# Kernel tuning notes

Measured on AMD Instinct MI355X. Metric: run time of the kernel, lower is better.

The kernel has to match this reference:

```python
import jax, jax.numpy as jnp
import numpy as np

N_HEADS = 16
N_KV_HEADS = 4
HEAD_DIM = 128
ROPE_BASE = 10000.0


def _rms_norm(x):
    eps = jnp.asarray(jnp.finfo(x.dtype).eps, x.dtype)
    return x * jax.lax.rsqrt(jnp.mean(x * x, axis=-1, keepdims=True) + eps)


def _rope_tables(T, dtype):
    d = HEAD_DIM
    inv_freq = 1.0 / (ROPE_BASE ** (jnp.arange(0, d, 2, dtype=jnp.float32) / d))
    freqs = jnp.outer(jnp.arange(T, dtype=jnp.float32), inv_freq)  # [T, d/2]
    return jnp.cos(freqs).astype(dtype), jnp.sin(freqs).astype(dtype)


def _apply_rope(x, cos, sin):
    # x: [B, H, T, D]; cos/sin: [T, D/2]
    d = x.shape[-1] // 2
    x1, x2 = x[..., :d], x[..., d:]
    return jnp.concatenate((x1 * cos + x2 * sin, -x1 * sin + x2 * cos), axis=-1)


def setup_inputs() -> dict:
    key = jax.random.key(0)
    ks = jax.random.split(key, 5)
    B, T, C = 2, 2048, 2048
    kv_dim = N_KV_HEADS * HEAD_DIM
    s = 0.02
    return {
        "x": jax.random.normal(ks[0], (B, T, C), jnp.float32),
        "Wq": jax.random.normal(ks[1], (C, C), jnp.float32) * s,
        "Wk": jax.random.normal(ks[2], (kv_dim, C), jnp.float32) * s,
        "Wv": jax.random.normal(ks[3], (kv_dim, C), jnp.float32) * s,
        "Wo": jax.random.normal(ks[4], (C, C), jnp.float32) * s,
    }


def reference(x, Wq, Wk, Wv, Wo):
    B, T, C = x.shape
    g = N_HEADS // N_KV_HEADS

    # QKV projections (torch Linear: x @ W.T), split into heads -> [B, H, T, D]
    q = (x @ Wq.T).reshape(B, T, N_HEADS, HEAD_DIM).transpose(0, 2, 1, 3)
    k = (x @ Wk.T).reshape(B, T, N_KV_HEADS, HEAD_DIM).transpose(0, 2, 1, 3)
    v = (x @ Wv.T).reshape(B, T, N_KV_HEADS, HEAD_DIM).transpose(0, 2, 1, 3)

    # QK RMSNorm (no learned weight)
    q, k = _rms_norm(q), _rms_norm(k)

    # RoPE
    cos, sin = _rope_tables(T, q.dtype)
    q, k = _apply_rope(q, cos, sin), _apply_rope(k, cos, sin)

    # GQA: expand kv heads
    k = jnp.repeat(k, g, axis=1)
    v = jnp.repeat(v, g, axis=1)

    # causal SDPA
    scale = 1.0 / jnp.sqrt(jnp.asarray(HEAD_DIM, q.dtype))
    scores = jnp.einsum("bhqd,bhkd->bhqk", q, k) * scale
    mask = jnp.tril(jnp.ones((T, T), bool))
    scores = jnp.where(mask, scores, jnp.asarray(-jnp.inf, scores.dtype))
    att = jax.nn.softmax(scores, axis=-1)
    y = jnp.einsum("bhqk,bhkd->bhqd", att, v)

    y = y.transpose(0, 2, 1, 3).reshape(B, T, C)
    return y @ Wo.T
```

## Files before the change

kernel.cpp:

```cpp
#include <hip/hip_runtime.h>
#include <hip/hip_bf16.h>
#include <cstdint>
#include <math.h>

#define DEVINL __device__ __forceinline__

typedef __attribute__((ext_vector_type(8))) __bf16 bf16x8;
typedef __attribute__((ext_vector_type(4))) float floatx4;

constexpr int TB = 2;
constexpr int TT = 2048;
constexpr int TC = 2048;
constexpr int NH = 16, NKV = 4, HD = 128;
constexpr int MR = TB * TT;
constexpr int NQ = NH * HD;
constexpr int NK = NKV * HD;
constexpr int NQKV = NQ + 2 * NK;

DEVINL unsigned bfbits(float f) {
  unsigned u = __builtin_bit_cast(unsigned, f);
  return (u + 0x7FFFu + ((u >> 16) & 1u)) >> 16;
}
DEVINL int pk2(float a, float b) {
  union { __hip_bfloat162 h; int i; } u;
  u.h = __float22bfloat162_rn(float2{a, b});
  return u.i;
}
DEVINL void gl_lds16(const __hip_bfloat16* g, __hip_bfloat16* l) {
  __builtin_amdgcn_global_load_lds(
      (const __attribute__((address_space(1))) unsigned int*)g,
      (__attribute__((address_space(3))) unsigned int*)l, 16, 0, 0);
}
DEVINL floatx4 mfma16(bf16x8 a, bf16x8 b, floatx4 c) {
  return __builtin_amdgcn_mfma_f32_16x16x32_bf16(a, b, c, 0, 0, 0);
}
DEVINL void cstore(float* p, float v) { *p = v; }
DEVINL void cstore(__hip_bfloat16* p, float v) { *(unsigned short*)p = (unsigned short)bfbits(v); }

__global__ __launch_bounds__(256) void k_cvt5(
    const float* __restrict__ s0, const float* __restrict__ s1,
    const float* __restrict__ s2, const float* __restrict__ s3,
    const float* __restrict__ s4,
    __hip_bfloat16* __restrict__ d0, __hip_bfloat16* __restrict__ d1,
    __hip_bfloat16* __restrict__ d2, __hip_bfloat16* __restrict__ d3,
    __hip_bfloat16* __restrict__ d4) {
  const float* s;
  __hip_bfloat16* d;
  int n;
  switch (blockIdx.y) {
    case 0: s = s0; d = d0; n = MR * TC; break;
    case 1: s = s1; d = d1; n = NQ * TC; break;
    case 2: s = s2; d = d2; n = NK * TC; break;
    case 3: s = s3; d = d3; n = NK * TC; break;
    default: s = s4; d = d4; n = TC * TC; break;
  }
  int i = (blockIdx.x * 256 + threadIdx.x) * 4;
  if (i >= n) return;
  float4 v = *(const float4*)(s + i);
  ushort4 o;
  o.x = (unsigned short)bfbits(v.x);
  o.y = (unsigned short)bfbits(v.y);
  o.z = (unsigned short)bfbits(v.z);
  o.w = (unsigned short)bfbits(v.w);
  *(ushort4*)(d + i) = o;
}

template <typename OUT_T>
__global__ __launch_bounds__(256, 2) void k_gemm_bt(
    const __hip_bfloat16* __restrict__ A, const __hip_bfloat16* __restrict__ B,
    OUT_T* __restrict__ C, int M, int N, int K) {
  __shared__ __align__(16) __hip_bfloat16 As[128 * 32];
  __shared__ __align__(16) __hip_bfloat16 Bs[128 * 32];
  const int tid = threadIdx.x;
  const int lane = tid & 63, w = tid >> 6;
  const int q15 = lane & 15, quad = lane >> 4;
  const int wm = w >> 1, wn = w & 1;
  const int tm = blockIdx.y, tn = blockIdx.x;

  const int r0 = tid >> 2, c0 = (tid & 3) * 8;
  const __hip_bfloat16* a0 = A + (size_t)(tm * 128 + r0) * K + c0;
  const __hip_bfloat16* a1 = A + (size_t)(tm * 128 + r0 + 64) * K + c0;
  const __hip_bfloat16* b0 = B + (size_t)(tn * 128 + r0) * K + c0;
  const __hip_bfloat16* b1 = B + (size_t)(tn * 128 + r0 + 64) * K + c0;
  __hip_bfloat16* lA0 = As + (tid & ~63) * 8;
  __hip_bfloat16* lA1 = As + 2048 + (tid & ~63) * 8;
  __hip_bfloat16* lB0 = Bs + (tid & ~63) * 8;
  __hip_bfloat16* lB1 = Bs + 2048 + (tid & ~63) * 8;

  floatx4 acc[4][4] = {};
  for (int k0 = 0; k0 < K; k0 += 32) {
    __syncthreads();
    gl_lds16(a0 + k0, lA0);
    gl_lds16(a1 + k0, lA1);
    gl_lds16(b0 + k0, lB0);
    gl_lds16(b1 + k0, lB1);
    __syncthreads();
    bf16x8 af[4], bfr[4];
#pragma unroll
    for (int i = 0; i < 4; i++)
      af[i] = *(const bf16x8*)(As + (wm * 64 + i * 16 + q15) * 32 + quad * 8);
#pragma unroll
    for (int i = 0; i < 4; i++)
      bfr[i] = *(const bf16x8*)(Bs + (wn * 64 + i * 16 + q15) * 32 + quad * 8);
#pragma unroll
    for (int mi = 0; mi < 4; mi++)
#pragma unroll
      for (int ni = 0; ni < 4; ni++)
        acc[mi][ni] = mfma16(af[mi], bfr[ni], acc[mi][ni]);
  }
#pragma unroll
  for (int mi = 0; mi < 4; mi++) {
    int row0 = tm * 128 + wm * 64 + mi * 16 + quad * 4;
#pragma unroll
    for (int ni = 0; ni < 4; ni++) {
      int col = tn * 128 + wn * 64 + ni * 16 + q15;
#pragma unroll
      for (int r = 0; r < 4; r++)
        cstore(C + (size_t)(row0 + r) * N + col, acc[mi][ni][r]);
    }
  }
}

constexpr int ROPE_BLOCKS = (MR * 20) / 4;
__global__ __launch_bounds__(256) void k_prep(
    const __hip_bfloat16* __restrict__ qkv,
    __hip_bfloat16* __restrict__ q_l, __hip_bfloat16* __restrict__ k_l,
    __hip_bfloat16* __restrict__ vt) {
  if (blockIdx.x < ROPE_BLOCKS) {
    int gw = (blockIdx.x * 256 + threadIdx.x) >> 6;
    int lane = threadIdx.x & 63;
    int head = gw % 20;
    int bt = gw / 20;
    int b = bt >> 11, t = bt & (TT - 1);
    bool isq = head < NH;
    int h = isq ? head : head - NH;
    const __hip_bfloat16* src = qkv + (size_t)bt * NQKV + (isq ? h * HD : NQ + h * HD);
    float x1 = __bfloat162float(src[lane]);
    float x2 = __bfloat162float(src[lane + 64]);
    float ss = x1 * x1 + x2 * x2;
#pragma unroll
    for (int m = 1; m < 64; m <<= 1) ss += __shfl_xor(ss, m, 64);
    float rinv = rsqrtf(ss * (1.0f / 128.0f) + 1.1920928955078125e-07f);
    float ang = (float)t * exp2f((float)lane * -(13.287712379549449f / 64.0f));
    float sv = sinf(ang), cv = cosf(ang);
    float scale = isq ? (1.4426950408889634f * 0.08838834764831845f) : 1.0f;
    float o1 = (x1 * cv + x2 * sv) * rinv * scale;
    float o2 = (x2 * cv - x1 * sv) * rinv * scale;
    __hip_bfloat16* dst = isq ? q_l + ((size_t)(b * NH + h) * TT + t) * HD
                              : k_l + ((size_t)(b * NKV + h) * TT + t) * HD;
    *(unsigned short*)(dst + lane) = (unsigned short)bfbits(o1);
    *(unsigned short*)(dst + lane + 64) = (unsigned short)bfbits(o2);
  } else {
    __shared__ __hip_bfloat16 tile[64][130];
    int bid = blockIdx.x - ROPE_BLOCKS;
    int t0 = (bid & 31) * 64;
    int hk = (bid >> 5) & 3;
    int b = bid >> 7;
    int tid = threadIdx.x;
#pragma unroll
    for (int j = 0; j < 32; j++) {
      int e = j * 256 + tid;
      int tt = e >> 7, d = e & 127;
      tile[tt][d] = qkv[(size_t)(b * TT + t0 + tt) * NQKV + NQ + NK + hk * HD + d];
    }
    __syncthreads();
#pragma unroll
    for (int j = 0; j < 32; j++) {
      int e = j * 256 + tid;
      int d = e >> 6, tt = e & 63;
      vt[(((size_t)(b * NKV + hk)) * HD + d) * TT + t0 + tt] = tile[tt][d];
    }
  }
}

__global__ __launch_bounds__(256, 2) void k_attn(
    const __hip_bfloat16* __restrict__ q_l, const __hip_bfloat16* __restrict__ k_l,
    const __hip_bfloat16* __restrict__ vt_l, __hip_bfloat16* __restrict__ y) {
  __shared__ __align__(16) __hip_bfloat16 Ks[2][64 * 128];
  __shared__ __align__(16) __hip_bfloat16 Vs[2][128 * 64];
  __shared__ __align__(16) __hip_bfloat16 Ps[4][32 * 64];
  const int tid = threadIdx.x, lane = tid & 63, w = tid >> 6;
  const int q15 = lane & 15, quad = lane >> 4;
  const int id = blockIdx.x;
  const int qt = (TT / 128 - 1) - (id >> 5);
  const int h = id & 15, b = (id >> 4) & 1;
  const int hk = h >> 2;
  const int nkb = 2 * qt + 2;

  const __hip_bfloat16* kbase = k_l + (size_t)(b * NKV + hk) * TT * HD;
  const __hip_bfloat16* vbase = vt_l + (size_t)(b * NKV + hk) * HD * TT;
  const __hip_bfloat16* qbase = q_l + ((size_t)(b * NH + h) * TT + qt * 128) * HD;

  auto stage = [&](int kb, int buf) {
#pragma unroll
    for (int i = 0; i < 4; i++) {
      int s = i * 256 + tid;
      int rk = s >> 4, ck = s & 15;
      gl_lds16(kbase + (size_t)(kb * 64 + rk) * HD + (ck ^ (rk & 15)) * 8,
               Ks[buf] + (i * 256 + (tid & ~63)) * 8);
      int rv = s >> 3, cv = s & 7;
      gl_lds16(vbase + (size_t)rv * TT + kb * 64 + (cv ^ (rv & 7)) * 8,
               Vs[buf] + (i * 256 + (tid & ~63)) * 8);
    }
  };

  bf16x8 qf[4][2];
#pragma unroll
  for (int dc = 0; dc < 4; dc++)
#pragma unroll
    for (int qh = 0; qh < 2; qh++)
      qf[dc][qh] = *(const bf16x8*)(qbase + (size_t)(w * 32 + qh * 16 + q15) * HD +
                                    dc * 32 + quad * 8);

  __hip_bfloat16* pw = Ps[w];
  const int qrow0 = q15, qrow1 = 16 + q15;
  const int pw_c = 2 * 0 + (quad >> 1);
  const int pw_h = (quad & 1) * 4;

  floatx4 ot[8][2] = {};
  float lsum[2] = {0.0f, 0.0f};
  int cur = 0;
  const int kb_last_w = 2 * qt + (w >> 1);

  for (int kb = 0; kb < nkb; kb++) {
    __syncthreads();
    if (kb == 0) {
      stage(0, cur);
      __syncthreads();
    }
    if (kb + 1 < nkb) stage(kb + 1, cur ^ 1);

    if (kb <= kb_last_w) {
      floatx4 st[4][2] = {};
#pragma unroll
      for (int kt = 0; kt < 4; kt++) {
        int r = kt * 16 + q15;
#pragma unroll
        for (int dc = 0; dc < 4; dc++) {
          int c = dc * 4 + quad;
          bf16x8 kf = *(const bf16x8*)(Ks[cur] + (r * 16 + (c ^ (r & 15))) * 8);
          st[kt][0] = mfma16(kf, qf[dc][0], st[kt][0]);
          st[kt][1] = mfma16(kf, qf[dc][1], st[kt][1]);
        }
      }
      if (kb >= 2 * qt) {
#pragma unroll
        for (int qh = 0; qh < 2; qh++) {
          int qg = qt * 128 + w * 32 + qh * 16 + q15;
#pragma unroll
          for (int kt = 0; kt < 4; kt++)
#pragma unroll
            for (int r = 0; r < 4; r++)
              if (kb * 64 + kt * 16 + quad * 4 + r > qg) st[kt][qh][r] = -INFINITY;
        }
      }
#pragma unroll
      for (int kt = 0; kt < 4; kt++) {
#pragma unroll
        for (int qh = 0; qh < 2; qh++) {
          float p0 = exp2f(st[kt][qh][0]);
          float p1 = exp2f(st[kt][qh][1]);
          float p2 = exp2f(st[kt][qh][2]);
          float p3 = exp2f(st[kt][qh][3]);
          lsum[qh] += (p0 + p1) + (p2 + p3);
          int2 pv;
          pv.x = pk2(p0, p1);
          pv.y = pk2(p2, p3);
          int row = qh * 16 + q15;
          int c4 = (kt * 2 + (quad >> 1)) ^ (row & 7);
          *(int2*)(pw + row * 64 + c4 * 8 + pw_h) = pv;
        }
      }
#pragma unroll
      for (int kc = 0; kc < 2; kc++) {
        bf16x8 pf[2];
#pragma unroll
        for (int qh = 0; qh < 2; qh++) {
          int row = qh * 16 + q15;
          int c4 = (kc * 4 + quad) ^ (row & 7);
          pf[qh] = *(const bf16x8*)(pw + row * 64 + c4 * 8);
        }
#pragma unroll
        for (int dt = 0; dt < 8; dt++) {
          int r = dt * 16 + q15, c = kc * 4 + quad;
          bf16x8 vf = *(const bf16x8*)(Vs[cur] + (r * 8 + (c ^ (r & 7))) * 8);
          ot[dt][0] = mfma16(vf, pf[0], ot[dt][0]);
          ot[dt][1] = mfma16(vf, pf[1], ot[dt][1]);
        }
      }
    }
    cur ^= 1;
  }
#pragma unroll
  for (int qh = 0; qh < 2; qh++) {
    float ls = lsum[qh];
    ls += __shfl_xor(ls, 16, 64);
    ls += __shfl_xor(ls, 32, 64);
    float linv = 1.0f / ls;
    int t = qt * 128 + w * 32 + qh * 16 + q15;
    __hip_bfloat16* yrow = y + (size_t)(b * TT + t) * TC + h * HD;
#pragma unroll
    for (int dt = 0; dt < 8; dt++) {
      int d = dt * 16 + quad * 4;
      ushort4 o;
      o.x = (unsigned short)bfbits(ot[dt][qh][0] * linv);
      o.y = (unsigned short)bfbits(ot[dt][qh][1] * linv);
      o.z = (unsigned short)bfbits(ot[dt][qh][2] * linv);
      o.w = (unsigned short)bfbits(ot[dt][qh][3] * linv);
      *(ushort4*)(yrow + d) = o;
    }
  }
}

extern "C" void kernel_launch(void* const* d_in, const int* in_sizes, int n_in,
                              void* d_out, int out_size, void* d_ws, size_t ws_size,
                              hipStream_t stream) {
  (void)in_sizes; (void)n_in; (void)out_size; (void)ws_size;
  const float* x  = (const float*)d_in[0];
  const float* Wq = (const float*)d_in[1];
  const float* Wk = (const float*)d_in[2];
  const float* Wv = (const float*)d_in[3];
  const float* Wo = (const float*)d_in[4];
  float* out = (float*)d_out;

  char* ws = (char*)d_ws;
  size_t off = 0;
  auto alloc = [&](size_t bytes) {
    void* p = ws + off;
    off += (bytes + 255) & ~(size_t)255;
    return p;
  };
  __hip_bfloat16* xb   = (__hip_bfloat16*)alloc((size_t)MR * TC * 2);
  __hip_bfloat16* wqkv = (__hip_bfloat16*)alloc((size_t)NQKV * TC * 2);
  __hip_bfloat16* wo   = (__hip_bfloat16*)alloc((size_t)TC * TC * 2);
  __hip_bfloat16* qkv  = (__hip_bfloat16*)alloc((size_t)MR * NQKV * 2);
  __hip_bfloat16* q_l  = (__hip_bfloat16*)alloc((size_t)TB * NH * TT * HD * 2);
  __hip_bfloat16* k_l  = (__hip_bfloat16*)alloc((size_t)TB * NKV * TT * HD * 2);
  __hip_bfloat16* vt_l = (__hip_bfloat16*)alloc((size_t)TB * NKV * HD * TT * 2);
  __hip_bfloat16* yb   = (__hip_bfloat16*)alloc((size_t)MR * TC * 2);

  k_cvt5<<<dim3((MR * TC / 4 + 255) / 256, 5), 256, 0, stream>>>(
      x, Wq, Wk, Wv, Wo,
      xb, wqkv, wqkv + (size_t)NQ * TC, wqkv + (size_t)(NQ + NK) * TC, wo);

  k_gemm_bt<__hip_bfloat16><<<dim3(NQKV / 128, MR / 128), 256, 0, stream>>>(
      xb, wqkv, qkv, MR, NQKV, TC);

  k_prep<<<ROPE_BLOCKS + TB * NKV * (TT / 64), 256, 0, stream>>>(qkv, q_l, k_l, vt_l);

  k_attn<<<(TT / 128) * NH * TB, 256, 0, stream>>>(q_l, k_l, vt_l, yb);

  k_gemm_bt<float><<<dim3(TC / 128, MR / 128), 256, 0, stream>>>(
      yb, wo, out, MR, TC, TC);
}
```

Before: 317.9 us.

## Switch attention to 32x32x16 MFMA with register-resident P via permlane swap

Result: slower. 330.9 us (+4.1%).

```diff
diff --git a/kernel.cpp b/kernel.cpp
--- a/kernel.cpp
+++ b/kernel.cpp
@@ -7,6 +7,8 @@
 
 typedef __attribute__((ext_vector_type(8))) __bf16 bf16x8;
 typedef __attribute__((ext_vector_type(4))) float floatx4;
+typedef __attribute__((ext_vector_type(16))) float floatx16;
+typedef __attribute__((ext_vector_type(4))) int intx4;
 
 constexpr int TB = 2;
 constexpr int TT = 2048;
@@ -33,6 +35,9 @@
 }
 DEVINL floatx4 mfma16(bf16x8 a, bf16x8 b, floatx4 c) {
   return __builtin_amdgcn_mfma_f32_16x16x32_bf16(a, b, c, 0, 0, 0);
+}
+DEVINL floatx16 mfma32(bf16x8 a, bf16x8 b, floatx16 c) {
+  return __builtin_amdgcn_mfma_f32_32x32x16_bf16(a, b, c, 0, 0, 0);
 }
 DEVINL void cstore(float* p, float v) { *p = v; }
 DEVINL void cstore(__hip_bfloat16* p, float v) { *(unsigned short*)p = (unsigned short)bfbits(v); }
@@ -178,9 +183,8 @@
     const __hip_bfloat16* __restrict__ vt_l, __hip_bfloat16* __restrict__ y) {
   __shared__ __align__(16) __hip_bfloat16 Ks[2][64 * 128];
   __shared__ __align__(16) __hip_bfloat16 Vs[2][128 * 64];
-  __shared__ __align__(16) __hip_bfloat16 Ps[4][32 * 64];
   const int tid = threadIdx.x, lane = tid & 63, w = tid >> 6;
-  const int q15 = lane & 15, quad = lane >> 4;
+  const int rq = lane & 31, hh = lane >> 5;
   const int id = blockIdx.x;
   const int qt = (TT / 128 - 1) - (id >> 5);
   const int h = id & 15, b = (id >> 4) & 1;
@@ -204,23 +208,20 @@
     }
   };
 
-  bf16x8 qf[4][2];
-#pragma unroll
-  for (int dc = 0; dc < 4; dc++)
-#pragma unroll
-    for (int qh = 0; qh < 2; qh++)
-      qf[dc][qh] = *(const bf16x8*)(qbase + (size_t)(w * 32 + qh * 16 + q15) * HD +
-                                    dc * 32 + quad * 8);
-
-  __hip_bfloat16* pw = Ps[w];
-  const int qrow0 = q15, qrow1 = 16 + q15;
-  const int pw_c = 2 * 0 + (quad >> 1);
-  const int pw_h = (quad & 1) * 4;
-
-  floatx4 ot[8][2] = {};
-  float lsum[2] = {0.0f, 0.0f};
+  bf16x8 qf[8];
+  {
+    const __hip_bfloat16* qrow = qbase + (size_t)(w * 32 + rq) * HD + hh * 8;
+#pragma unroll
+    for (int m = 0; m < 8; m++) qf[m] = *(const bf16x8*)(qrow + m * 16);
+  }
+
+  floatx16 ot[4] = {};
+  float lsum = 0.0f;
   int cur = 0;
-  const int kb_last_w = 2 * qt + (w >> 1);
+  const int qg = qt * 128 + w * 32 + rq;
+  const int qminw = qt * 128 + w * 32;
+  const int qmaxw = qminw + 31;
+  const int kb_last_w = qmaxw >> 6;
 
   for (int kb = 0; kb < nkb; kb++) {
     __syncthreads();
@@ -231,85 +232,72 @@
     if (kb + 1 < nkb) stage(kb + 1, cur ^ 1);
 
     if (kb <= kb_last_w) {
-      floatx4 st[4][2] = {};
-#pragma unroll
-      for (int kt = 0; kt < 4; kt++) {
-        int r = kt * 16 + q15;
-#pragma unroll
-        for (int dc = 0; dc < 4; dc++) {
-          int c = dc * 4 + quad;
-          bf16x8 kf = *(const bf16x8*)(Ks[cur] + (r * 16 + (c ^ (r & 15))) * 8);
-          st[kt][0] = mfma16(kf, qf[dc][0], st[kt][0]);
-          st[kt][1] = mfma16(kf, qf[dc][1], st[kt][1]);
+#pragma unroll
+      for (int t = 0; t < 2; t++) {
+        if (kb * 64 + t * 32 > qmaxw) continue;
+        floatx16 st = {};
+        __builtin_amdgcn_s_setprio(1);
+#pragma unroll
+        for (int m = 0; m < 8; m++) {
+          bf16x8 kf = *(const bf16x8*)(Ks[cur] + (t * 32 + rq) * 128 +
+                                       (((2 * m + hh) ^ (rq & 15)) * 8));
+          st = mfma32(kf, qf[m], st);
         }
+        __builtin_amdgcn_s_setprio(0);
+        const bool nm = (kb * 64 + t * 32 + 31) > qminw;
+        bf16x8 pf[2];
+#pragma unroll
+        for (int g = 0; g < 2; g++) {
+          float p[8];
+#pragma unroll
+          for (int e = 0; e < 8; e++) {
+            float sv = st[8 * g + e];
+            if (nm) {
+              int kg = kb * 64 + t * 32 + 16 * g + (e & 3) + 8 * (e >> 2) + 4 * hh;
+              if (kg > qg) sv = -INFINITY;
+            }
+            p[e] = exp2f(sv);
+          }
+          lsum += ((p[0] + p[1]) + (p[2] + p[3])) + ((p[4] + p[5]) + (p[6] + p[7]));
+          int a0 = pk2(p[0], p[1]), a1 = pk2(p[2], p[3]);
+          int b0 = pk2(p[4], p[5]), b1 = pk2(p[6], p[7]);
+          asm("v_permlane32_swap_b32 %0, %1" : "+v"(a0), "+v"(b0));
+          asm("v_permlane32_swap_b32 %0, %1" : "+v"(a1), "+v"(b1));
+          intx4 w4;
+          w4[0] = a0; w4[1] = a1; w4[2] = b0; w4[3] = b1;
+          pf[g] = __builtin_bit_cast(bf16x8, w4);
+        }
+        __builtin_amdgcn_s_setprio(1);
+#pragma unroll
+        for (int g = 0; g < 2; g++)
+#pragma unroll
+          for (int dt = 0; dt < 4; dt++) {
+            bf16x8 vf = *(const bf16x8*)(Vs[cur] + (dt * 32 + rq) * 64 +
+                                         (((4 * t + 2 * g + hh) ^ (rq & 7)) * 8));
+            ot[dt] = mfma32(vf, pf[g], ot[dt]);
+          }
+        __builtin_amdgcn_s_setprio(0);
       }
-      if (kb >= 2 * qt) {
-#pragma unroll
-        for (int qh = 0; qh < 2; qh++) {
-          int qg = qt * 128 + w * 32 + qh * 16 + q15;
-#pragma unroll
-          for (int kt = 0; kt < 4; kt++)
-#pragma unroll
-            for (int r = 0; r < 4; r++)
-              if (kb * 64 + kt * 16 + quad * 4 + r > qg) st[kt][qh][r] = -INFINITY;
-        }
-      }
-#pragma unroll
-      for (int kt = 0; kt < 4; kt++) {
-#pragma unroll
-        for (int qh = 0; qh < 2; qh++) {
-          float p0 = exp2f(st[kt][qh][0]);
-          float p1 = exp2f(st[kt][qh][1]);
-          float p2 = exp2f(st[kt][qh][2]);
-          float p3 = exp2f(st[kt][qh][3]);
-          lsum[qh] += (p0 + p1) + (p2 + p3);
-          int2 pv;
-          pv.x = pk2(p0, p1);
-          pv.y = pk2(p2, p3);
-          int row = qh * 16 + q15;
-          int c4 = (kt * 2 + (quad >> 1)) ^ (row & 7);
-          *(int2*)(pw + row * 64 + c4 * 8 + pw_h) = pv;
-        }
-      }
-#pragma unroll
-      for (int kc = 0; kc < 2; kc++) {
-        bf16x8 pf[2];
-#pragma unroll
-        for (int qh = 0; qh < 2; qh++) {
-          int row = qh * 16 + q15;
-          int c4 = (kc * 4 + quad) ^ (row & 7);
-          pf[qh] = *(const bf16x8*)(pw + row * 64 + c4 * 8);
-        }
-#pragma unroll
-        for (int dt = 0; dt < 8; dt++) {
-          int r = dt * 16 + q15, c = kc * 4 + quad;
-          bf16x8 vf = *(const bf16x8*)(Vs[cur] + (r * 8 + (c ^ (r & 7))) * 8);
-          ot[dt][0] = mfma16(vf, pf[0], ot[dt][0]);
-          ot[dt][1] = mfma16(vf, pf[1], ot[dt][1]);
-        }
-      }
     }
     cur ^= 1;
   }
-#pragma unroll
-  for (int qh = 0; qh < 2; qh++) {
-    float ls = lsum[qh];
-    ls += __shfl_xor(ls, 16, 64);
-    ls += __shfl_xor(ls, 32, 64);
-    float linv = 1.0f / ls;
-    int t = qt * 128 + w * 32 + qh * 16 + q15;
-    __hip_bfloat16* yrow = y + (size_t)(b * TT + t) * TC + h * HD;
-#pragma unroll
-    for (int dt = 0; dt < 8; dt++) {
-      int d = dt * 16 + quad * 4;
+
+  float lt = lsum + __shfl_xor(lsum, 32, 64);
+  float linv = 1.0f / lt;
+  const int trow = qt * 128 + w * 32 + rq;
+  __hip_bfloat16* yrow = y + (size_t)(b * TT + trow) * TC + h * HD;
+#pragma unroll
+  for (int dt = 0; dt < 4; dt++)
+#pragma unroll
+    for (int rg = 0; rg < 4; rg++) {
+      int d0 = dt * 32 + rg * 8 + 4 * hh;
       ushort4 o;
-      o.x = (unsigned short)bfbits(ot[dt][qh][0] * linv);
-      o.y = (unsigned short)bfbits(ot[dt][qh][1] * linv);
-      o.z = (unsigned short)bfbits(ot[dt][qh][2] * linv);
-      o.w = (unsigned short)bfbits(ot[dt][qh][3] * linv);
-      *(ushort4*)(yrow + d) = o;
-    }
-  }
+      o.x = (unsigned short)bfbits(ot[dt][4 * rg + 0] * linv);
+      o.y = (unsigned short)bfbits(ot[dt][4 * rg + 1] * linv);
+      o.z = (unsigned short)bfbits(ot[dt][4 * rg + 2] * linv);
+      o.w = (unsigned short)bfbits(ot[dt][4 * rg + 3] * linv);
+      *(ushort4*)(yrow + d0) = o;
+    }
 }
 
 extern "C" void kernel_launch(void* const* d_in, const int* in_sizes, int n_in,
```

## Double GEMM K-tile to 64 with XOR-swizzled LDS layout

Applied to the files above, without the earlier changes.

After: 310.7 us. -2.3%, faster.

```diff
diff --git a/kernel.cpp b/kernel.cpp
--- a/kernel.cpp
+++ b/kernel.cpp
@@ -69,44 +69,47 @@
 __global__ __launch_bounds__(256, 2) void k_gemm_bt(
     const __hip_bfloat16* __restrict__ A, const __hip_bfloat16* __restrict__ B,
     OUT_T* __restrict__ C, int M, int N, int K) {
-  __shared__ __align__(16) __hip_bfloat16 As[128 * 32];
-  __shared__ __align__(16) __hip_bfloat16 Bs[128 * 32];
+  __shared__ __align__(16) __hip_bfloat16 As[128 * 64];
+  __shared__ __align__(16) __hip_bfloat16 Bs[128 * 64];
   const int tid = threadIdx.x;
   const int lane = tid & 63, w = tid >> 6;
   const int q15 = lane & 15, quad = lane >> 4;
   const int wm = w >> 1, wn = w & 1;
   const int tm = blockIdx.y, tn = blockIdx.x;
 
-  const int r0 = tid >> 2, c0 = (tid & 3) * 8;
-  const __hip_bfloat16* a0 = A + (size_t)(tm * 128 + r0) * K + c0;
-  const __hip_bfloat16* a1 = A + (size_t)(tm * 128 + r0 + 64) * K + c0;
-  const __hip_bfloat16* b0 = B + (size_t)(tn * 128 + r0) * K + c0;
-  const __hip_bfloat16* b1 = B + (size_t)(tn * 128 + r0 + 64) * K + c0;
-  __hip_bfloat16* lA0 = As + (tid & ~63) * 8;
-  __hip_bfloat16* lA1 = As + 2048 + (tid & ~63) * 8;
-  __hip_bfloat16* lB0 = Bs + (tid & ~63) * 8;
-  __hip_bfloat16* lB1 = Bs + 2048 + (tid & ~63) * 8;
+  const int r0 = tid >> 3;
+  const int csw = ((tid & 7) ^ (r0 & 7)) * 8;
+  const __hip_bfloat16* ag = A + (size_t)(tm * 128 + r0) * K + csw;
+  const __hip_bfloat16* bg = B + (size_t)(tn * 128 + r0) * K + csw;
+  __hip_bfloat16* lA = As + (tid & ~63) * 8;
+  __hip_bfloat16* lB = Bs + (tid & ~63) * 8;
 
   floatx4 acc[4][4] = {};
-  for (int k0 = 0; k0 < K; k0 += 32) {
+  for (int k0 = 0; k0 < K; k0 += 64) {
     __syncthreads();
-    gl_lds16(a0 + k0, lA0);
-    gl_lds16(a1 + k0, lA1);
-    gl_lds16(b0 + k0, lB0);
-    gl_lds16(b1 + k0, lB1);
+#pragma unroll
+    for (int i = 0; i < 4; i++) {
+      gl_lds16(ag + (size_t)(i * 32) * K + k0, lA + i * 2048);
+      gl_lds16(bg + (size_t)(i * 32) * K + k0, lB + i * 2048);
+    }
     __syncthreads();
-    bf16x8 af[4], bfr[4];
-#pragma unroll
-    for (int i = 0; i < 4; i++)
-      af[i] = *(const bf16x8*)(As + (wm * 64 + i * 16 + q15) * 32 + quad * 8);
-#pragma unroll
-    for (int i = 0; i < 4; i++)
-      bfr[i] = *(const bf16x8*)(Bs + (wn * 64 + i * 16 + q15) * 32 + quad * 8);
-#pragma unroll
-    for (int mi = 0; mi < 4; mi++)
-#pragma unroll
-      for (int ni = 0; ni < 4; ni++)
-        acc[mi][ni] = mfma16(af[mi], bfr[ni], acc[mi][ni]);
+#pragma unroll
+    for (int kh = 0; kh < 2; kh++) {
+      bf16x8 af[4], bfr[4];
+#pragma unroll
+      for (int i = 0; i < 4; i++)
+        af[i] = *(const bf16x8*)(As + (wm * 64 + i * 16 + q15) * 64 +
+                                 (((kh * 4 + quad) ^ (q15 & 7)) * 8));
+#pragma unroll
+      for (int i = 0; i < 4; i++)
+        bfr[i] = *(const bf16x8*)(Bs + (wn * 64 + i * 16 + q15) * 64 +
+                                  (((kh * 4 + quad) ^ (q15 & 7)) * 8));
+#pragma unroll
+      for (int mi = 0; mi < 4; mi++)
+#pragma unroll
+        for (int ni = 0; ni < 4; ni++)
+          acc[mi][ni] = mfma16(af[mi], bfr[ni], acc[mi][ni]);
+    }
   }
 #pragma unroll
   for (int mi = 0; mi < 4; mi++) {
```
